# Optimization experiments

Measured on AMD Instinct MI355X. Metric: run time of the kernel, lower is better.

Reference implementation:

```python
import jax, jax.numpy as jnp
import numpy as np

N, D, H, C, E = 50000, 128, 4, 32, 600000  # C = D // H
LRELU_SLOPE = 0.2
EPS_LN = 1e-5
EPS_SOFTMAX = 1e-16


def layer_norm(x, g, b):
    m = jnp.mean(x, axis=-1, keepdims=True)
    v = jnp.mean((x - m) ** 2, axis=-1, keepdims=True)
    return (x - m) * jax.lax.rsqrt(v + EPS_LN) * g + b


def setup_inputs() -> dict:
    key = jax.random.key(0)
    ks = jax.random.split(key, 10)
    glorot = lambda k, shape: jax.random.normal(k, shape, jnp.float32) * np.sqrt(2.0 / (shape[0] + shape[-1]))
    return {
        "x": jax.random.normal(ks[0], (N, D), jnp.float32),
        "edge_index": jax.random.randint(ks[1], (2, E), 0, N, jnp.int32),
        "edge_attr": jax.random.uniform(ks[2], (E,), jnp.float32),
        "timestamps": jax.random.uniform(ks[3], (E,), jnp.float32),
        "W_gat": glorot(ks[4], (D, H * C)),
        "att_src": glorot(ks[5], (H, C)),
        "att_dst": glorot(ks[6], (H, C)),
        "bias_gat": jnp.zeros((H * C,), jnp.float32),
        "ln1_g": jnp.ones((D,), jnp.float32),
        "ln1_b": jnp.zeros((D,), jnp.float32),
        "ln2_g": jnp.ones((D,), jnp.float32),
        "ln2_b": jnp.zeros((D,), jnp.float32),
    }


def reference(x, edge_index, edge_attr, timestamps, W_gat, att_src, att_dst,
              bias_gat, ln1_g, ln1_b, ln2_g, ln2_b):
    n = x.shape[0]
    # TemporalAttention is just LayerNorm(x)
    xt = layer_norm(x, ln1_g, ln1_b)

    # GATConv with default add_self_loops=True, concat=True, dropout=0 (eval)
    loop = jnp.arange(n, dtype=edge_index.dtype)
    src = jnp.concatenate([edge_index[0], loop])  # [E+N]
    dst = jnp.concatenate([edge_index[1], loop])  # aggregation target

    h = (xt @ W_gat).reshape(n, H, C)            # [N,H,C]
    a_src = jnp.sum(h * att_src, axis=-1)        # [N,H]
    a_dst = jnp.sum(h * att_dst, axis=-1)        # [N,H]

    alpha = jax.nn.leaky_relu(a_src[src] + a_dst[dst], LRELU_SLOPE)  # [E+N,H]
    amax = jax.ops.segment_max(alpha, dst, num_segments=n)
    alpha = jnp.exp(alpha - amax[dst])
    asum = jax.ops.segment_sum(alpha, dst, num_segments=n)
    alpha = alpha / (asum[dst] + EPS_SOFTMAX)

    msg = h[src] * alpha[:, :, None]             # [E+N,H,C]
    out = jax.ops.segment_sum(msg, dst, num_segments=n).reshape(n, H * C) + bias_gat

    # residual + LayerNorm (dropout is identity in eval)
    return layer_norm(xt + out, ln2_g, ln2_b)
```

## Files before the change

kernel.cpp:

```cpp
#include <hip/hip_runtime.h>
#include <hip/hip_bf16.h>

typedef unsigned short u16;
typedef unsigned int u32;
typedef __attribute__((ext_vector_type(8))) short short8;
typedef __attribute__((ext_vector_type(4))) float f32x4;

#define LRELU_SLOPE 0.2f
#define EPS_LN 1e-5f
#define EPS_SM 1e-16f
#define SCAN_CHUNK 4096
#define NBLK 256

__device__ __forceinline__ float bflo(u32 u){ union{u32 i; float f;} x; x.i = u<<16; return x.f; }
__device__ __forceinline__ float bfhi(u32 u){ union{u32 i; float f;} x; x.i = u & 0xffff0000u; return x.f; }
__device__ __forceinline__ float bf1(u16 u){ union{u32 i; float f;} x; x.i = ((u32)u)<<16; return x.f; }
__device__ __forceinline__ u16 f2bf(float f){
  union{float f; u32 i;} x; x.f=f; u32 i=x.i;
  u32 r = (i + 0x7fffu + ((i>>16)&1u))>>16; return (u16)r;
}
__device__ __forceinline__ u32 pack2(float a, float b){ return (u32)f2bf(a) | ((u32)f2bf(b)<<16); }
__device__ __forceinline__ float lrelu(float x){ return x > 0.f ? x : LRELU_SLOPE*x; }

__device__ __forceinline__ float wsum(float v){
  #pragma unroll
  for(int o=32;o>0;o>>=1) v += __shfl_xor(v,o,64);
  return v;
}

__global__ __launch_bounds__(256) void ln1_kernel(const float* __restrict__ x,
    const float* __restrict__ g, const float* __restrict__ b,
    u16* __restrict__ xt, int n){
  int row  = blockIdx.x*4 + (threadIdx.x>>6);
  int lane = threadIdx.x & 63;
  if(row >= n) return;
  float2 xv = ((const float2*)(x + (size_t)row*128))[lane];
  float v0 = xv.x, v1 = xv.y;
  float mean = wsum(v0+v1) * (1.f/128.f);
  float d0 = v0-mean, d1 = v1-mean;
  float var = wsum(d0*d0 + d1*d1) * (1.f/128.f);
  float rstd = rsqrtf(var + EPS_LN);
  float2 gv = ((const float2*)g)[lane], bv = ((const float2*)b)[lane];
  float o0 = d0*rstd*gv.x + bv.x;
  float o1 = d1*rstd*gv.y + bv.y;
  ((u32*)(xt + (size_t)row*128))[lane] = pack2(o0, o1);
}

__global__ __launch_bounds__(256) void gemm_kernel(const u16* __restrict__ xt,
    const float* __restrict__ W, const float* __restrict__ att_src, const float* __restrict__ att_dst,
    u16* __restrict__ h, float* __restrict__ a_src, float* __restrict__ a_dst, int n){
  __shared__ u16 Wf[16384];
  __shared__ u16 Xb[64*136];
  int tid = threadIdx.x;
  int r0  = blockIdx.x*64;

  const float4* W4 = (const float4*)W;
  for(int p=tid; p<2048; p+=256){
    int g = p & 31, kk = p >> 5;
    int k0 = kk*2, n0 = g*4;
    float4 w0 = W4[k0*32 + g];
    float4 w1 = W4[(k0+1)*32 + g];
    int ks = k0>>5, q = (k0>>3)&3, j = k0&7;
    float e0[4] = {w0.x,w0.y,w0.z,w0.w};
    float e1[4] = {w1.x,w1.y,w1.z,w1.w};
    #pragma unroll
    for(int u=0;u<4;u++){
      int nn = n0+u;
      int idx = (((nn>>4)*4 + ks)*64 + q*16 + (nn&15))*8 + j;
      ((u32*)Wf)[idx>>1] = pack2(e0[u], e1[u]);
    }
  }
  for(int i=tid; i<1024; i+=256){
    int row = i>>4, seg = i&15;
    int gr = r0+row;
    uint4 v = (gr<n) ? ((const uint4*)(xt + (size_t)gr*128))[seg] : make_uint4(0,0,0,0);
    *(uint4*)&Xb[row*136 + seg*8] = v;
  }
  __syncthreads();

  int w = tid>>6, lane = tid&63;
  int slab = w*16, c = lane&15, q = lane>>4;
  f32x4 acc[8];
  #pragma unroll
  for(int t=0;t<8;t++) acc[t] = (f32x4){0.f,0.f,0.f,0.f};
  #pragma unroll
  for(int ks=0;ks<4;ks++){
    short8 A = *(const short8*)&Xb[(slab + c)*136 + ks*32 + q*8];
    #pragma unroll
    for(int t=0;t<8;t++){
      short8 B = *(const short8*)&Wf[((t*4+ks)*64 + lane)*8];
      acc[t] = __builtin_amdgcn_mfma_f32_16x16x32_bf16(A, B, acc[t], 0, 0, 0);
    }
  }
  __syncthreads();
  #pragma unroll
  for(int t=0;t<8;t++){
    #pragma unroll
    for(int r=0;r<4;r++){
      Xb[(slab + q*4 + r)*136 + t*16 + c] = f2bf(acc[t][r]);
    }
  }
  __syncthreads();
  {
    int row = tid>>2, qt = tid&3;
    int gr = r0+row;
    if(gr<n){
      const uint4* src = (const uint4*)((const char*)Xb + row*272 + qt*64);
      uint4* dst = (uint4*)((char*)(h + (size_t)gr*128) + qt*64);
      dst[0] = src[0];
      dst[1] = src[1];
      dst[2] = src[2];
      dst[3] = src[3];
    }
    int hd = qt;
    if(gr<n){
      float as=0.f, ad=0.f;
      const u16* hp = &Xb[row*136 + hd*32];
      #pragma unroll
      for(int sgm=0;sgm<4;sgm++){
        #pragma unroll
        for(int e=0;e<8;e++){
          float v = bf1(hp[sgm*8+e]);
          as = fmaf(v, att_src[hd*32+sgm*8+e], as);
          ad = fmaf(v, att_dst[hd*32+sgm*8+e], ad);
        }
      }
      a_src[(size_t)gr*4+hd] = as;
      a_dst[(size_t)gr*4+hd] = ad;
    }
  }
}

__global__ __launch_bounds__(256) void binA_kernel(const int* __restrict__ dst,
    int* __restrict__ bhT, int E, int CH, int NB){
  __shared__ u32 hist[512];
  int tid = threadIdx.x, i = blockIdx.x;
  for(int b=tid; b<NB; b+=256) hist[b]=0;
  __syncthreads();
  int e0=i*CH, e1=min(E, e0+CH);
  for(int e=e0+tid; e<e1; e+=256) atomicAdd(&hist[(u32)dst[e]>>7], 1u);
  __syncthreads();
  for(int b=tid; b<NB; b+=256) bhT[b*NBLK + i] = (int)hist[b];
}

__global__ __launch_bounds__(256) void scanA_kernel(const int* __restrict__ deg,
    int* __restrict__ pref, int* __restrict__ bsum, int n){
  __shared__ int part[256];
  int tid = threadIdx.x;
  int base = blockIdx.x*SCAN_CHUNK + tid*16;
  int v[16]; int s=0;
  #pragma unroll
  for(int i=0;i<16;i++){ int idx=base+i; int xv=(idx<n)? deg[idx]:0; v[i]=s; s+=xv; }
  part[tid]=s; __syncthreads();
  int mys=s;
  for(int off=1;off<256;off<<=1){
    int t = (tid>=off)? part[tid-off] : 0;
    __syncthreads(); part[tid]+=t; __syncthreads();
  }
  int run = part[tid]-mys;
  #pragma unroll
  for(int i=0;i<16;i++){
    int idx=base+i;
    if(idx<=n) pref[idx]=v[i]+run;
  }
  if(tid==255) bsum[blockIdx.x]=part[255];
}
__global__ __launch_bounds__(64) void scanB_kernel(int* __restrict__ bsum, int nb){
  int lane = threadIdx.x;
  int v = (lane<nb)? bsum[lane] : 0;
  int inc = v;
  #pragma unroll
  for(int o=1;o<64;o<<=1){ int t=__shfl_up(inc,o,64); if(lane>=o) inc+=t; }
  if(lane<nb) bsum[lane] = inc - v;
}

__global__ __launch_bounds__(256) void binC_kernel(const int* __restrict__ src,
    const int* __restrict__ dst, const int* __restrict__ bhpref, const int* __restrict__ bsum2,
    u32* __restrict__ ebuf, int E, int CH, int NB){
  __shared__ u32 cur[512];
  int tid = threadIdx.x, i = blockIdx.x;
  for(int b=tid; b<NB; b+=256){
    int j = b*NBLK + i;
    cur[b] = (u32)(bhpref[j] + bsum2[j>>12]);
  }
  __syncthreads();
  int e0=i*CH, e1=min(E, e0+CH);
  for(int e=e0+tid; e<e1; e+=256){
    u32 s = (u32)src[e], d = (u32)dst[e];
    u32 pos = atomicAdd(&cur[d>>7], 1u);
    ebuf[pos] = s | ((d & 127u) << 16);
  }
}

__global__ __launch_bounds__(256) void binD_kernel(const u32* __restrict__ ebuf,
    const int* __restrict__ bhpref, const int* __restrict__ bsum2,
    int* __restrict__ rowptr, u16* __restrict__ col, int n, int E){
  __shared__ int cnt[128], cur[128];
  int tid = threadIdx.x, b = blockIdx.x;
  int j0 = b*NBLK, j1 = (b+1)*NBLK;
  int base = bhpref[j0] + bsum2[j0>>12];
  int end  = bhpref[j1] + bsum2[j1>>12];
  int cb = end - base;
  if(tid<128) cnt[tid]=0;
  __syncthreads();
  for(int k=tid; k<cb; k+=256) atomicAdd(&cnt[(ebuf[base+k]>>16)&127], 1);
  __syncthreads();
  for(int o=1;o<128;o<<=1){
    int t = (tid>=o && tid<128)? cnt[tid-o] : 0;
    __syncthreads();
    if(tid<128) cnt[tid]+=t;
    __syncthreads();
  }
  int nd = min(128, n - (b<<7));
  if(tid<128){
    int excl = tid? cnt[tid-1] : 0;
    cur[tid] = excl;
    if(tid<nd) rowptr[(b<<7)+tid] = base + excl;
  }
  if(b==0 && tid==0) rowptr[n] = E;
  __syncthreads();
  for(int k=tid; k<cb; k+=256){
    u32 v = ebuf[base+k];
    int l = (int)((v>>16)&127u);
    int p = atomicAdd(&cur[l], 1);
    col[base+p] = (u16)(v & 0xffffu);
  }
}

__global__ __launch_bounds__(256) void agg_kernel(const u16* __restrict__ h,
    const float* __restrict__ a_src, const float* __restrict__ a_dst,
    const int* __restrict__ rowptr, const u16* __restrict__ col,
    const u16* __restrict__ xt, const float* __restrict__ bias,
    const float* __restrict__ g2, const float* __restrict__ b2,
    float* __restrict__ out, int n){
  int lane = threadIdx.x & 63;
  int wv   = threadIdx.x >> 6;
  int g    = lane >> 4;
  int li   = lane & 15;
  int hc   = li >> 2;
  int d    = blockIdx.x*16 + wv*4 + g;
  bool dok = d < n;
  int dc   = dok ? d : (n-1);

  float4 ad  = ((const float4*)a_dst)[dc];
  float4 asd = ((const float4*)a_src)[dc];
  float ad_h = hc==0? ad.x  : hc==1? ad.y  : hc==2? ad.z  : ad.w;
  float as_h = hc==0? asd.x : hc==1? asd.y : hc==2? asd.z : asd.w;
  float t_h  = __expf(fminf(lrelu(as_h + ad_h), 60.f));

  int base = rowptr[dc];
  int end  = rowptr[dc+1];
  int deg  = dok ? (end - base) : 0;
  int dm = deg;
  dm = max(dm, __shfl_xor(dm, 16, 64));
  dm = max(dm, __shfl_xor(dm, 32, 64));

  float p0=0.f,p1=0.f,p2=0.f,p3=0.f;
  float acc[8]={};
  for(int j0=0;j0<dm;j0+=16){
    int j = j0 + li;
    bool vv = j < deg;
    int sx = vv ? (int)col[base+j] : 0;
    float4 a = ((const float4*)a_src)[sx];
    float y0 = vv ? __expf(fminf(lrelu(a.x+ad.x),60.f)) : 0.f;
    float y1 = vv ? __expf(fminf(lrelu(a.y+ad.y),60.f)) : 0.f;
    float y2 = vv ? __expf(fminf(lrelu(a.z+ad.z),60.f)) : 0.f;
    float y3 = vv ? __expf(fminf(lrelu(a.w+ad.w),60.f)) : 0.f;
    p0+=y0; p1+=y1; p2+=y2; p3+=y3;
    int ccm = min(dm - j0, 16);
    int gbase = g<<4;
    for(int jj=0; jj<ccm; jj++){
      int srcl = gbase + jj;
      float f0=__shfl(y0,srcl,64), f1=__shfl(y1,srcl,64);
      float f2=__shfl(y2,srcl,64), f3=__shfl(y3,srcl,64);
      int   sj=__shfl(sx,srcl,64);
      float al = hc==0? f0 : hc==1? f1 : hc==2? f2 : f3;
      uint4 hv = *(const uint4*)(h + (size_t)sj*128 + li*8);
      acc[0]=fmaf(al,bflo(hv.x),acc[0]); acc[1]=fmaf(al,bfhi(hv.x),acc[1]);
      acc[2]=fmaf(al,bflo(hv.y),acc[2]); acc[3]=fmaf(al,bfhi(hv.y),acc[3]);
      acc[4]=fmaf(al,bflo(hv.z),acc[4]); acc[5]=fmaf(al,bfhi(hv.z),acc[5]);
      acc[6]=fmaf(al,bflo(hv.w),acc[6]); acc[7]=fmaf(al,bfhi(hv.w),acc[7]);
    }
  }
  #pragma unroll
  for(int o=1;o<16;o<<=1){
    p0+=__shfl_xor(p0,o,64); p1+=__shfl_xor(p1,o,64);
    p2+=__shfl_xor(p2,o,64); p3+=__shfl_xor(p3,o,64);
  }
  float den = (hc==0? p0 : hc==1? p1 : hc==2? p2 : p3) + t_h + EPS_SM;
  uint4 hd4 = *(const uint4*)(h + (size_t)dc*128 + li*8);
  acc[0]=fmaf(t_h,bflo(hd4.x),acc[0]); acc[1]=fmaf(t_h,bfhi(hd4.x),acc[1]);
  acc[2]=fmaf(t_h,bflo(hd4.y),acc[2]); acc[3]=fmaf(t_h,bfhi(hd4.y),acc[3]);
  acc[4]=fmaf(t_h,bflo(hd4.z),acc[4]); acc[5]=fmaf(t_h,bfhi(hd4.z),acc[5]);
  acc[6]=fmaf(t_h,bflo(hd4.w),acc[6]); acc[7]=fmaf(t_h,bfhi(hd4.w),acc[7]);
  float inv = 1.f/den;

  uint4 xv4 = *(const uint4*)(xt + (size_t)dc*128 + li*8);
  const float* bp = bias + li*8;
  float4 ba = *(const float4*)bp, bb = *(const float4*)(bp+4);
  float r[8];
  r[0]=bflo(xv4.x)+acc[0]*inv+ba.x; r[1]=bfhi(xv4.x)+acc[1]*inv+ba.y;
  r[2]=bflo(xv4.y)+acc[2]*inv+ba.z; r[3]=bfhi(xv4.y)+acc[3]*inv+ba.w;
  r[4]=bflo(xv4.z)+acc[4]*inv+bb.x; r[5]=bfhi(xv4.z)+acc[5]*inv+bb.y;
  r[6]=bflo(xv4.w)+acc[6]*inv+bb.z; r[7]=bfhi(xv4.w)+acc[7]*inv+bb.w;
  float part=0;
  #pragma unroll
  for(int c=0;c<8;c++) part+=r[c];
  #pragma unroll
  for(int o=1;o<16;o<<=1) part += __shfl_xor(part,o,64);
  float mean = part*(1.f/128.f);
  float vp=0;
  #pragma unroll
  for(int c=0;c<8;c++){ float dd=r[c]-mean; vp+=dd*dd; }
  #pragma unroll
  for(int o=1;o<16;o<<=1) vp += __shfl_xor(vp,o,64);
  float var = vp*(1.f/128.f);
  float rstd = rsqrtf(var+EPS_LN);
  const float* gp = g2 + li*8; const float* b2p = b2 + li*8;
  float4 ga = *(const float4*)gp,  gb = *(const float4*)(gp+4);
  float4 c2a= *(const float4*)b2p, c2b= *(const float4*)(b2p+4);
  if(dok){
    float* op = out + (size_t)d*128 + li*8;
    float4 o0 = make_float4((r[0]-mean)*rstd*ga.x+c2a.x, (r[1]-mean)*rstd*ga.y+c2a.y,
                            (r[2]-mean)*rstd*ga.z+c2a.z, (r[3]-mean)*rstd*ga.w+c2a.w);
    float4 o1 = make_float4((r[4]-mean)*rstd*gb.x+c2b.x, (r[5]-mean)*rstd*gb.y+c2b.y,
                            (r[6]-mean)*rstd*gb.z+c2b.z, (r[7]-mean)*rstd*gb.w+c2b.w);
    *(float4*)op     = o0;
    *(float4*)(op+4) = o1;
  }
}

extern "C" void kernel_launch(void* const* d_in, const int* in_sizes, int n_in,
                              void* d_out, int out_size, void* d_ws, size_t ws_size,
                              hipStream_t stream) {
  const float* x     = (const float*)d_in[0];
  const int*   ei    = (const int*)d_in[1];
  const float* W     = (const float*)d_in[4];
  const float* att_s = (const float*)d_in[5];
  const float* att_d = (const float*)d_in[6];
  const float* bias  = (const float*)d_in[7];
  const float* g1    = (const float*)d_in[8];
  const float* b1    = (const float*)d_in[9];
  const float* g2    = (const float*)d_in[10];
  const float* b2    = (const float*)d_in[11];
  int n = in_sizes[0]/128;
  int E = in_sizes[1]/2;
  float* out = (float*)d_out;

  int NB = (n+127)>>7;
  int CH = (E + NBLK - 1)/NBLK;
  int NH = NB*NBLK;
  int nb2 = NH/SCAN_CHUNK + 1;

  char* ws = (char*)d_ws;
  u16*   xt     = (u16*)ws;   ws += (size_t)n*128*2;
  u16*   h      = (u16*)ws;   ws += (size_t)n*128*2;
  float* a_src  = (float*)ws; ws += (size_t)n*4*4;
  float* a_dst  = (float*)ws; ws += (size_t)n*4*4;
  int*   rowptr = (int*)ws;   ws += (((size_t)(n+1)*4 + 255) & ~(size_t)255);
  u16*   col    = (u16*)ws;   ws += (((size_t)E*2 + 255) & ~(size_t)255);
  char* hs = (char*)h;
  u32*   ebuf   = (u32*)hs;                 hs += (size_t)E*4;
  int*   bhT    = (int*)hs;                 hs += (size_t)NH*4;
  int*   bhpref = (int*)hs;                 hs += (((size_t)(NH+1)*4 + 255) & ~(size_t)255);
  int*   bsum2  = (int*)hs;

  dim3 b256(256);
  ln1_kernel  <<<(n+3)/4,   b256, 0, stream>>>(x, g1, b1, xt, n);
  binA_kernel <<<NBLK,      b256, 0, stream>>>(ei+E, bhT, E, CH, NB);
  scanA_kernel<<<nb2,       b256, 0, stream>>>(bhT, bhpref, bsum2, NH);
  scanB_kernel<<<1,         64,   0, stream>>>(bsum2, nb2);
  binC_kernel <<<NBLK,      b256, 0, stream>>>(ei, ei+E, bhpref, bsum2, ebuf, E, CH, NB);
  binD_kernel <<<NB,        b256, 0, stream>>>(ebuf, bhpref, bsum2, rowptr, col, n, E);
  gemm_kernel <<<(n+63)/64, b256, 0, stream>>>(xt, W, att_s, att_d, h, a_src, a_dst, n);
  agg_kernel  <<<(n+15)/16, b256, 0, stream>>>(h, a_src, a_dst, rowptr, col, xt, bias, g2, b2, out, n);
}
```

Measured before the change: 191.4 us.

## Fuse binning stages into LN1 and GEMM kernels, use LDS broadcast in aggregation

Folds the destination histogram into the LayerNorm kernel, moves the block-sum scan into the scatter and bucket-sort consumers, and merges the per-bucket CSR sort into the GEMM kernel. The launch count drops from eight to five. The scratch buffers move out of the aliased h region into their own workspace so the sort and the GEMM can run in the same kernel without clobbering h. The aggregation inner loop now stages edge weights and source indices in LDS instead of using five shuffles per edge, and it loops to each group's own degree. The risks are that the fused blocks get longer tails and that the extra LDS could lower occupancy.

```diff
diff --git a/kernel.cpp b/kernel.cpp
--- a/kernel.cpp
+++ b/kernel.cpp
@@ -28,32 +28,139 @@
   return v;
 }
 
-__global__ __launch_bounds__(256) void ln1_kernel(const float* __restrict__ x,
+__global__ __launch_bounds__(256) void ln1A_kernel(const float* __restrict__ x,
     const float* __restrict__ g, const float* __restrict__ b,
-    u16* __restrict__ xt, int n){
-  int row  = blockIdx.x*4 + (threadIdx.x>>6);
-  int lane = threadIdx.x & 63;
-  if(row >= n) return;
-  float2 xv = ((const float2*)(x + (size_t)row*128))[lane];
-  float v0 = xv.x, v1 = xv.y;
-  float mean = wsum(v0+v1) * (1.f/128.f);
-  float d0 = v0-mean, d1 = v1-mean;
-  float var = wsum(d0*d0 + d1*d1) * (1.f/128.f);
-  float rstd = rsqrtf(var + EPS_LN);
-  float2 gv = ((const float2*)g)[lane], bv = ((const float2*)b)[lane];
-  float o0 = d0*rstd*gv.x + bv.x;
-  float o1 = d1*rstd*gv.y + bv.y;
-  ((u32*)(xt + (size_t)row*128))[lane] = pack2(o0, o1);
-}
-
-__global__ __launch_bounds__(256) void gemm_kernel(const u16* __restrict__ xt,
+    u16* __restrict__ xt, int n,
+    const int* __restrict__ edst, int* __restrict__ bhT, int E, int CH, int NB){
+  __shared__ u32 hist[512];
+  int tid = threadIdx.x;
+  bool doA = blockIdx.x < NBLK;
+  if(doA){ for(int bb=tid; bb<NB; bb+=256) hist[bb]=0u; }
+
+  int row  = blockIdx.x*4 + (tid>>6);
+  int lane = tid & 63;
+  if(row < n){
+    float2 xv = ((const float2*)(x + (size_t)row*128))[lane];
+    float v0 = xv.x, v1 = xv.y;
+    float mean = wsum(v0+v1) * (1.f/128.f);
+    float d0 = v0-mean, d1 = v1-mean;
+    float var = wsum(d0*d0 + d1*d1) * (1.f/128.f);
+    float rstd = rsqrtf(var + EPS_LN);
+    float2 gv = ((const float2*)g)[lane], bv = ((const float2*)b)[lane];
+    float o0 = d0*rstd*gv.x + bv.x;
+    float o1 = d1*rstd*gv.y + bv.y;
+    ((u32*)(xt + (size_t)row*128))[lane] = pack2(o0, o1);
+  }
+  if(doA){
+    __syncthreads();
+    int i = blockIdx.x;
+    int e0=i*CH, e1=min(E, e0+CH);
+    for(int e=e0+tid; e<e1; e+=256) atomicAdd(&hist[(u32)edst[e]>>7], 1u);
+    __syncthreads();
+    for(int bb=tid; bb<NB; bb+=256) bhT[bb*NBLK + i] = (int)hist[bb];
+  }
+}
+
+__global__ __launch_bounds__(256) void scanA_kernel(const int* __restrict__ deg,
+    int* __restrict__ pref, int* __restrict__ bsum, int n){
+  __shared__ int part[256];
+  int tid = threadIdx.x;
+  int base = blockIdx.x*SCAN_CHUNK + tid*16;
+  int v[16]; int s=0;
+  #pragma unroll
+  for(int i=0;i<16;i++){ int idx=base+i; int xv=(idx<n)? deg[idx]:0; v[i]=s; s+=xv; }
+  part[tid]=s; __syncthreads();
+  int mys=s;
+  for(int off=1;off<256;off<<=1){
+    int t = (tid>=off)? part[tid-off] : 0;
+    __syncthreads(); part[tid]+=t; __syncthreads();
+  }
+  int run = part[tid]-mys;
+  #pragma unroll
+  for(int i=0;i<16;i++){
+    int idx=base+i;
+    if(idx<=n) pref[idx]=v[i]+run;
+  }
+  if(tid==255) bsum[blockIdx.x]=part[255];
+}
+
+__global__ __launch_bounds__(256) void binC_kernel(const int* __restrict__ src,
+    const int* __restrict__ dst, const int* __restrict__ bhpref, const int* __restrict__ bsum2,
+    u32* __restrict__ ebuf, int E, int CH, int NB, int nb2){
+  __shared__ u32 cur[512];
+  __shared__ int boff[64];
+  int tid = threadIdx.x, i = blockIdx.x;
+  if(tid<64){
+    int v = (tid<nb2)? bsum2[tid] : 0;
+    int inc = v;
+    #pragma unroll
+    for(int o=1;o<64;o<<=1){ int t=__shfl_up(inc,o,64); if(tid>=o) inc+=t; }
+    boff[tid] = inc - v;
+  }
+  __syncthreads();
+  for(int bb=tid; bb<NB; bb+=256){
+    int j = bb*NBLK + i;
+    cur[bb] = (u32)(bhpref[j] + boff[j>>12]);
+  }
+  __syncthreads();
+  int e0=i*CH, e1=min(E, e0+CH);
+  for(int e=e0+tid; e<e1; e+=256){
+    u32 s = (u32)src[e], d = (u32)dst[e];
+    u32 pos = atomicAdd(&cur[d>>7], 1u);
+    ebuf[pos] = s | ((d & 127u) << 16);
+  }
+}
+
+__global__ __launch_bounds__(256) void gemmD_kernel(const u16* __restrict__ xt,
     const float* __restrict__ W, const float* __restrict__ att_src, const float* __restrict__ att_dst,
-    u16* __restrict__ h, float* __restrict__ a_src, float* __restrict__ a_dst, int n){
+    u16* __restrict__ h, float* __restrict__ a_src, float* __restrict__ a_dst, int n,
+    const u32* __restrict__ ebuf, const int* __restrict__ bhpref, const int* __restrict__ bsum2,
+    int* __restrict__ rowptr, u16* __restrict__ col, int NB, int nb2, int E){
   __shared__ u16 Wf[16384];
   __shared__ u16 Xb[64*136];
+  __shared__ int dcnt[128], dcur[128], dboff[64];
   int tid = threadIdx.x;
-  int r0  = blockIdx.x*64;
-
+
+  if(blockIdx.x < (u32)NB){
+    int bkt = blockIdx.x;
+    if(tid<64){
+      int v = (tid<nb2)? bsum2[tid] : 0;
+      int inc = v;
+      #pragma unroll
+      for(int o=1;o<64;o<<=1){ int t=__shfl_up(inc,o,64); if(tid>=o) inc+=t; }
+      dboff[tid] = inc - v;
+    }
+    if(tid<128) dcnt[tid]=0;
+    __syncthreads();
+    int j0 = bkt*NBLK, j1 = (bkt+1)*NBLK;
+    int base = bhpref[j0] + dboff[j0>>12];
+    int end  = bhpref[j1] + dboff[j1>>12];
+    int cb = end - base;
+    for(int k=tid; k<cb; k+=256) atomicAdd(&dcnt[(ebuf[base+k]>>16)&127], 1);
+    __syncthreads();
+    for(int o=1;o<128;o<<=1){
+      int t = (tid>=o && tid<128)? dcnt[tid-o] : 0;
+      __syncthreads();
+      if(tid<128) dcnt[tid]+=t;
+      __syncthreads();
+    }
+    int nd = min(128, n - (bkt<<7));
+    if(tid<128){
+      int excl = tid? dcnt[tid-1] : 0;
+      dcur[tid] = excl;
+      if(tid<nd) rowptr[(bkt<<7)+tid] = base + excl;
+    }
+    if(bkt==0 && tid==0) rowptr[n] = E;
+    __syncthreads();
+    for(int k=tid; k<cb; k+=256){
+      u32 v = ebuf[base+k];
+      int l = (int)((v>>16)&127u);
+      int p = atomicAdd(&dcur[l], 1);
+      col[base+p] = (u16)(v & 0xffffu);
+    }
+  }
+
+  int r0 = blockIdx.x*64;
   const float4* W4 = (const float4*)W;
   for(int p=tid; p<2048; p+=256){
     int g = p & 31, kk = p >> 5;
@@ -131,114 +238,23 @@
   }
 }
 
-__global__ __launch_bounds__(256) void binA_kernel(const int* __restrict__ dst,
-    int* __restrict__ bhT, int E, int CH, int NB){
-  __shared__ u32 hist[512];
-  int tid = threadIdx.x, i = blockIdx.x;
-  for(int b=tid; b<NB; b+=256) hist[b]=0;
-  __syncthreads();
-  int e0=i*CH, e1=min(E, e0+CH);
-  for(int e=e0+tid; e<e1; e+=256) atomicAdd(&hist[(u32)dst[e]>>7], 1u);
-  __syncthreads();
-  for(int b=tid; b<NB; b+=256) bhT[b*NBLK + i] = (int)hist[b];
-}
-
-__global__ __launch_bounds__(256) void scanA_kernel(const int* __restrict__ deg,
-    int* __restrict__ pref, int* __restrict__ bsum, int n){
-  __shared__ int part[256];
-  int tid = threadIdx.x;
-  int base = blockIdx.x*SCAN_CHUNK + tid*16;
-  int v[16]; int s=0;
-  #pragma unroll
-  for(int i=0;i<16;i++){ int idx=base+i; int xv=(idx<n)? deg[idx]:0; v[i]=s; s+=xv; }
-  part[tid]=s; __syncthreads();
-  int mys=s;
-  for(int off=1;off<256;off<<=1){
-    int t = (tid>=off)? part[tid-off] : 0;
-    __syncthreads(); part[tid]+=t; __syncthreads();
-  }
-  int run = part[tid]-mys;
-  #pragma unroll
-  for(int i=0;i<16;i++){
-    int idx=base+i;
-    if(idx<=n) pref[idx]=v[i]+run;
-  }
-  if(tid==255) bsum[blockIdx.x]=part[255];
-}
-__global__ __launch_bounds__(64) void scanB_kernel(int* __restrict__ bsum, int nb){
-  int lane = threadIdx.x;
-  int v = (lane<nb)? bsum[lane] : 0;
-  int inc = v;
-  #pragma unroll
-  for(int o=1;o<64;o<<=1){ int t=__shfl_up(inc,o,64); if(lane>=o) inc+=t; }
-  if(lane<nb) bsum[lane] = inc - v;
-}
-
-__global__ __launch_bounds__(256) void binC_kernel(const int* __restrict__ src,
-    const int* __restrict__ dst, const int* __restrict__ bhpref, const int* __restrict__ bsum2,
-    u32* __restrict__ ebuf, int E, int CH, int NB){
-  __shared__ u32 cur[512];
-  int tid = threadIdx.x, i = blockIdx.x;
-  for(int b=tid; b<NB; b+=256){
-    int j = b*NBLK + i;
-    cur[b] = (u32)(bhpref[j] + bsum2[j>>12]);
-  }
-  __syncthreads();
-  int e0=i*CH, e1=min(E, e0+CH);
-  for(int e=e0+tid; e<e1; e+=256){
-    u32 s = (u32)src[e], d = (u32)dst[e];
-    u32 pos = atomicAdd(&cur[d>>7], 1u);
-    ebuf[pos] = s | ((d & 127u) << 16);
-  }
-}
-
-__global__ __launch_bounds__(256) void binD_kernel(const u32* __restrict__ ebuf,
-    const int* __restrict__ bhpref, const int* __restrict__ bsum2,
-    int* __restrict__ rowptr, u16* __restrict__ col, int n, int E){
-  __shared__ int cnt[128], cur[128];
-  int tid = threadIdx.x, b = blockIdx.x;
-  int j0 = b*NBLK, j1 = (b+1)*NBLK;
-  int base = bhpref[j0] + bsum2[j0>>12];
-  int end  = bhpref[j1] + bsum2[j1>>12];
-  int cb = end - base;
-  if(tid<128) cnt[tid]=0;
-  __syncthreads();
-  for(int k=tid; k<cb; k+=256) atomicAdd(&cnt[(ebuf[base+k]>>16)&127], 1);
-  __syncthreads();
-  for(int o=1;o<128;o<<=1){
-    int t = (tid>=o && tid<128)? cnt[tid-o] : 0;
-    __syncthreads();
-    if(tid<128) cnt[tid]+=t;
-    __syncthreads();
-  }
-  int nd = min(128, n - (b<<7));
-  if(tid<128){
-    int excl = tid? cnt[tid-1] : 0;
-    cur[tid] = excl;
-    if(tid<nd) rowptr[(b<<7)+tid] = base + excl;
-  }
-  if(b==0 && tid==0) rowptr[n] = E;
-  __syncthreads();
-  for(int k=tid; k<cb; k+=256){
-    u32 v = ebuf[base+k];
-    int l = (int)((v>>16)&127u);
-    int p = atomicAdd(&cur[l], 1);
-    col[base+p] = (u16)(v & 0xffffu);
-  }
-}
-
 __global__ __launch_bounds__(256) void agg_kernel(const u16* __restrict__ h,
     const float* __restrict__ a_src, const float* __restrict__ a_dst,
     const int* __restrict__ rowptr, const u16* __restrict__ col,
     const u16* __restrict__ xt, const float* __restrict__ bias,
     const float* __restrict__ g2, const float* __restrict__ b2,
     float* __restrict__ out, int n){
+  __shared__ float ybuf[16*68];
+  __shared__ int   sxbuf[16*17];
   int lane = threadIdx.x & 63;
   int wv   = threadIdx.x >> 6;
   int g    = lane >> 4;
   int li   = lane & 15;
   int hc   = li >> 2;
-  int d    = blockIdx.x*16 + wv*4 + g;
+  int gid  = wv*4 + g;
+  float* yb = ybuf  + gid*68;
+  int*   sb = sxbuf + gid*17;
+  int d    = blockIdx.x*16 + gid;
   bool dok = d < n;
   int dc   = dok ? d : (n-1);
 
@@ -249,8 +265,7 @@
   float t_h  = __expf(fminf(lrelu(as_h + ad_h), 60.f));
 
   int base = rowptr[dc];
-  int end  = rowptr[dc+1];
-  int deg  = dok ? (end - base) : 0;
+  int deg  = dok ? (rowptr[dc+1] - base) : 0;
   int dm = deg;
   dm = max(dm, __shfl_xor(dm, 16, 64));
   dm = max(dm, __shfl_xor(dm, 32, 64));
@@ -267,20 +282,20 @@
     float y2 = vv ? __expf(fminf(lrelu(a.z+ad.z),60.f)) : 0.f;
     float y3 = vv ? __expf(fminf(lrelu(a.w+ad.w),60.f)) : 0.f;
     p0+=y0; p1+=y1; p2+=y2; p3+=y3;
-    int ccm = min(dm - j0, 16);
-    int gbase = g<<4;
+    *(float4*)&yb[li*4] = make_float4(y0,y1,y2,y3);
+    sb[li] = sx;
+    __builtin_amdgcn_sched_barrier(0);
+    int ccm = min(deg - j0, 16);
     for(int jj=0; jj<ccm; jj++){
-      int srcl = gbase + jj;
-      float f0=__shfl(y0,srcl,64), f1=__shfl(y1,srcl,64);
-      float f2=__shfl(y2,srcl,64), f3=__shfl(y3,srcl,64);
-      int   sj=__shfl(sx,srcl,64);
-      float al = hc==0? f0 : hc==1? f1 : hc==2? f2 : f3;
+      float al = yb[jj*4 + hc];
+      int   sj = sb[jj];
       uint4 hv = *(const uint4*)(h + (size_t)sj*128 + li*8);
       acc[0]=fmaf(al,bflo(hv.x),acc[0]); acc[1]=fmaf(al,bfhi(hv.x),acc[1]);
       acc[2]=fmaf(al,bflo(hv.y),acc[2]); acc[3]=fmaf(al,bfhi(hv.y),acc[3]);
       acc[4]=fmaf(al,bflo(hv.z),acc[4]); acc[5]=fmaf(al,bfhi(hv.z),acc[5]);
       acc[6]=fmaf(al,bflo(hv.w),acc[6]); acc[7]=fmaf(al,bfhi(hv.w),acc[7]);
     }
+    __builtin_amdgcn_sched_barrier(0);
   }
   #pragma unroll
   for(int o=1;o<16;o<<=1){
@@ -347,9 +362,9 @@
   int E = in_sizes[1]/2;
   float* out = (float*)d_out;
 
-  int NB = (n+127)>>7;
-  int CH = (E + NBLK - 1)/NBLK;
-  int NH = NB*NBLK;
+  int NB  = (n+127)>>7;
+  int CH  = (E + NBLK - 1)/NBLK;
+  int NH  = NB*NBLK;
   int nb2 = NH/SCAN_CHUNK + 1;
 
   char* ws = (char*)d_ws;
@@ -359,19 +374,16 @@
   float* a_dst  = (float*)ws; ws += (size_t)n*4*4;
   int*   rowptr = (int*)ws;   ws += (((size_t)(n+1)*4 + 255) & ~(size_t)255);
   u16*   col    = (u16*)ws;   ws += (((size_t)E*2 + 255) & ~(size_t)255);
-  char* hs = (char*)h;
-  u32*   ebuf   = (u32*)hs;                 hs += (size_t)E*4;
-  int*   bhT    = (int*)hs;                 hs += (size_t)NH*4;
-  int*   bhpref = (int*)hs;                 hs += (((size_t)(NH+1)*4 + 255) & ~(size_t)255);
-  int*   bsum2  = (int*)hs;
+  u32*   ebuf   = (u32*)ws;   ws += (size_t)E*4;
+  int*   bhT    = (int*)ws;   ws += (size_t)NH*4;
+  int*   bhpref = (int*)ws;   ws += (((size_t)(NH+1)*4 + 255) & ~(size_t)255);
+  int*   bsum2  = (int*)ws;   ws += 256*4;
 
   dim3 b256(256);
-  ln1_kernel  <<<(n+3)/4,   b256, 0, stream>>>(x, g1, b1, xt, n);
-  binA_kernel <<<NBLK,      b256, 0, stream>>>(ei+E, bhT, E, CH, NB);
+  ln1A_kernel <<<(n+3)/4,   b256, 0, stream>>>(x, g1, b1, xt, n, ei+E, bhT, E, CH, NB);
   scanA_kernel<<<nb2,       b256, 0, stream>>>(bhT, bhpref, bsum2, NH);
-  scanB_kernel<<<1,         64,   0, stream>>>(bsum2, nb2);
-  binC_kernel <<<NBLK,      b256, 0, stream>>>(ei, ei+E, bhpref, bsum2, ebuf, E, CH, NB);
-  binD_kernel <<<NB,        b256, 0, stream>>>(ebuf, bhpref, bsum2, rowptr, col, n, E);
-  gemm_kernel <<<(n+63)/64, b256, 0, stream>>>(xt, W, att_s, att_d, h, a_src, a_dst, n);
+  binC_kernel <<<NBLK,      b256, 0, stream>>>(ei, ei+E, bhpref, bsum2, ebuf, E, CH, NB, nb2);
+  gemmD_kernel<<<(n+63)/64, b256, 0, stream>>>(xt, W, att_s, att_d, h, a_src, a_dst, n,
+                                               ebuf, bhpref, bsum2, rowptr, col, NB, nb2, E);
   agg_kernel  <<<(n+15)/16, b256, 0, stream>>>(h, a_src, a_dst, rowptr, col, xt, bias, g2, b2, out, n);
 }
```

Measured after the change: 175.7 us. 8.2% less time.
